# Kernel tuning notes

Hardware: AMD Instinct MI355X
Metric: run time of the kernel (lower is better)

## Reference

```python
import jax, jax.numpy as jnp
import numpy as np

# Dims matching init_kwargs: k=5, inplanes=512, planes=512, m=4, padding=None, stride=1
N, C, H, W = 32, 512, 56, 56
M = 4
CM = C // M          # 128, = group count (depthwise)
K1 = 5               # dynamic kernel size
K2 = 3               # atrous kernel size (dilation 2)
P2 = 512 // 2        # planes // 2


def setup_inputs() -> dict:
    key = jax.random.key(0)
    ks = jax.random.split(key, 13)
    s = lambda i, shape: jax.random.normal(ks[i], shape, jnp.float32) * 0.05
    return dict(
        x=jax.random.normal(ks[0], (N, C, H, W), jnp.float32),
        W_conv=s(1, (CM, C)), b_conv=s(2, (CM,)),        # self.conv (1x1)
        wk=s(3, (K1 * K1,)), bk=s(4, (K1 * K1,)),        # self.conv_kernel (1->k*k, 1x1)
        wck=s(5, ()), bck=s(6, ()),                      # self.conv_k (1->1, 1x1 scalar affine)
        wk2=s(7, (K2 * K2,)), bk2=s(8, (K2 * K2,)),      # self.conv_kernel2 (1->9)
        wck2=s(9, ()), bck2=s(10, ()),                   # self.conv_k2
        W_fuse=s(11, (P2, CM)), b_fuse=s(12, (P2,)),     # self.fuse (1x1)
    )


def _dw_conv(f, kern, dil, pad):
    # Per-sample depthwise conv: fold batch into groups -> single conv call.
    # f: [N, CM, H, W], kern: [N, CM, k, k]
    n, cm, h, w = f.shape
    fr = f.reshape(1, n * cm, h, w)
    kr = kern.reshape(n * cm, 1, kern.shape[-2], kern.shape[-1])
    o = jax.lax.conv_general_dilated(
        fr, kr, window_strides=(1, 1), padding=[(pad, pad), (pad, pad)],
        rhs_dilation=(dil, dil), feature_group_count=n * cm,
        dimension_numbers=('NCHW', 'OIHW', 'NCHW'))
    return o.reshape(n, cm, h, w)


def reference(x, W_conv, b_conv, wk, bk, wck, bck, wk2, bk2, wck2, bck2, W_fuse, b_fuse):
    # f = relu(conv(x));  g = relu(conv(avg_pool(x)))
    f = jax.nn.relu(jnp.einsum('nchw,oc->nohw', x, W_conv) + b_conv[None, :, None, None])
    g = jax.nn.relu(x.mean((2, 3)) @ W_conv.T + b_conv)  # [N, CM]
    # dynamic per-channel kernels: (g*wk + bk)*wck + bck, reshaped to [N, CM, k, k]
    kern1 = ((g[:, :, None] * wk + bk) * wck + bck).reshape(N, CM, K1, K1)
    kern2 = ((g[:, :, None] * wk2 + bk2) * wck2 + bck2).reshape(N, CM, K2, K2)
    o1 = _dw_conv(f, kern1, dil=1, pad=(K1 - 1) // 2)   # plain branch
    o2 = _dw_conv(f, kern2, dil=2, pad=2)               # atrous branch
    y1 = jnp.einsum('nchw,oc->nohw', o1, W_fuse) + b_fuse[None, :, None, None]
    y2 = jnp.einsum('nchw,oc->nohw', o2, W_fuse) + b_fuse[None, :, None, None]
    return jnp.concatenate([y1, y2], axis=1)  # [N, planes, H, W]
```

## Files before the change

kernel.cpp:

```cpp
#include <hip/hip_runtime.h>

typedef unsigned short u16;
typedef unsigned int   u32;

#define NB   32
#define CIN  512
#define CM   128
#define P2   256
#define HW   3136
#define HD   56

typedef __attribute__((ext_vector_type(8))) short           short8;
typedef __attribute__((ext_vector_type(8))) unsigned short  ushort8;
typedef __attribute__((ext_vector_type(4))) unsigned short  ushort4_t;
typedef __attribute__((ext_vector_type(4))) float           f32x4;

__device__ __forceinline__ float b2f(u16 u) {
    union { u32 i; float f; } v; v.i = ((u32)u) << 16; return v.f;
}
__device__ __forceinline__ u16 f2b(float f) {
    u32 u = __builtin_bit_cast(u32, f);
    u32 r = (u + 0x7fffu + ((u >> 16) & 1u)) >> 16;
    return (u16)r;
}

__global__ __launch_bounds__(256) void init_kernel(const float* __restrict__ Wc,
                                                   const float* __restrict__ Wf,
                                                   u16* __restrict__ Wcb,
                                                   u16* __restrict__ Wfb,
                                                   float* __restrict__ xm) {
    int i = blockIdx.x * 256 + threadIdx.x;
    if (i < CM * CIN) { Wcb[i] = f2b(Wc[i]); return; }
    i -= CM * CIN;
    if (i < P2 * CM) { Wfb[i] = f2b(Wf[i]); return; }
    i -= P2 * CM;
    if (i < NB * CIN) xm[i] = 0.f;
}

__global__ __launch_bounds__(128) void g_kernel(const float* __restrict__ Wc,
                                                const float* __restrict__ bc,
                                                const float* __restrict__ xm,
                                                float* __restrict__ g) {
    const int n = blockIdx.x, cm = threadIdx.x;
    __shared__ float xs[CIN];
    for (int i = threadIdx.x; i < CIN; i += 128)
        xs[i] = xm[n * CIN + i] * (1.0f / HW);
    __syncthreads();
    const float* wrow = Wc + (size_t)cm * CIN;
    float acc = 0.f;
    for (int c = 0; c < CIN; ++c) acc += wrow[c] * xs[c];
    acc += bc[cm];
    g[n * CM + cm] = fmaxf(acc, 0.f);
}

template<int IN_F32, int OUT_F32, int RELU, int MEAN, int TWOBR>
__global__ __launch_bounds__(256) void gemm_kernel(
    const void* __restrict__ In0, const void* __restrict__ In1,
    const u16* __restrict__ Wm, const float* __restrict__ bias,
    void* __restrict__ Out, float* __restrict__ xm,
    int K, int ch_stride)
{
    __shared__ u16 ldsT[128 * 36];

    int n, ch_off;
    const void* In;
    if (TWOBR) {
        n      = blockIdx.z >> 1;
        int br = blockIdx.z & 1;
        In     = br ? In1 : In0;
        ch_off = br ? P2 : 0;
    } else {
        n = blockIdx.z; In = In0; ch_off = 0;
    }
    const int hw0  = blockIdx.x * 128;
    const int mblk = blockIdx.y * 128;
    const int tid  = threadIdx.x;
    const int wave = tid >> 6, lane = tid & 63;
    const int wm   = (wave >> 1) * 64;
    const int wn   = (wave & 1) * 64;
    const int qa   = lane >> 4;
    const int l15  = lane & 15;

    f32x4 acc[4][4] = {};

    const int kpair = tid >> 4;
    const int c0    = (tid & 15) * 8;
    const int hwc   = hw0 + c0;
    const bool cok  = (hwc < HW);

    for (int k0 = 0; k0 < K; k0 += 32) {
        __syncthreads();
        u32 pk[8];
        if (IN_F32) {
            f32x4 a0 = {0,0,0,0}, a1 = {0,0,0,0}, d0 = {0,0,0,0}, d1 = {0,0,0,0};
            if (cok) {
                const float* p0 = (const float*)In + (size_t)n * K * HW
                                + (size_t)(k0 + kpair * 2) * HW + hwc;
                a0 = *(const f32x4*)p0;
                a1 = *(const f32x4*)(p0 + 4);
                d0 = *(const f32x4*)(p0 + HW);
                d1 = *(const f32x4*)(p0 + HW + 4);
            }
            float fa[8] = {a0[0],a0[1],a0[2],a0[3],a1[0],a1[1],a1[2],a1[3]};
            float fb[8] = {d0[0],d0[1],d0[2],d0[3],d1[0],d1[1],d1[2],d1[3]};
            #pragma unroll
            for (int e = 0; e < 8; ++e) {
                u32 ua = __builtin_bit_cast(u32, fa[e]) + 0x8000u;
                u32 ub = __builtin_bit_cast(u32, fb[e]) + 0x8000u;
                pk[e] = __builtin_amdgcn_perm(ub, ua, 0x07060302u);
            }
            if (MEAN) {
                float s0 = fa[0]+fa[1]+fa[2]+fa[3]+fa[4]+fa[5]+fa[6]+fa[7];
                float s1 = fb[0]+fb[1]+fb[2]+fb[3]+fb[4]+fb[5]+fb[6]+fb[7];
                #pragma unroll
                for (int off = 8; off > 0; off >>= 1) {
                    s0 += __shfl_xor(s0, off, 16);
                    s1 += __shfl_xor(s1, off, 16);
                }
                if ((tid & 15) == 0) {
                    atomicAdd(&xm[n * CIN + k0 + kpair * 2],     s0);
                    atomicAdd(&xm[n * CIN + k0 + kpair * 2 + 1], s1);
                }
            }
        } else {
            ushort8 v0 = {0,0,0,0,0,0,0,0}, v1 = {0,0,0,0,0,0,0,0};
            if (cok) {
                const u16* p0 = (const u16*)In + (size_t)n * K * HW
                              + (size_t)(k0 + kpair * 2) * HW + hwc;
                v0 = *(const ushort8*)p0;
                v1 = *(const ushort8*)(p0 + HW);
            }
            #pragma unroll
            for (int e = 0; e < 8; ++e)
                pk[e] = (u32)v0[e] | ((u32)v1[e] << 16);
        }
        #pragma unroll
        for (int e = 0; e < 8; ++e)
            *(u32*)&ldsT[(c0 + e) * 36 + kpair * 2] = pk[e];
        __syncthreads();

        short8 a[4];
        #pragma unroll
        for (int mt = 0; mt < 4; ++mt) {
            int row = mblk + wm + mt * 16 + l15;
            a[mt] = *(const short8*)(Wm + (size_t)row * K + k0 + qa * 8);
        }
        #pragma unroll
        for (int nt = 0; nt < 4; ++nt) {
            int c = wn + nt * 16 + l15;
            union { ushort4_t h[2]; short8 v; } bu;
            bu.h[0] = *(const ushort4_t*)&ldsT[c * 36 + qa * 8];
            bu.h[1] = *(const ushort4_t*)&ldsT[c * 36 + qa * 8 + 4];
            short8 b = bu.v;
            #pragma unroll
            for (int mt = 0; mt < 4; ++mt)
                acc[mt][nt] = __builtin_amdgcn_mfma_f32_16x16x32_bf16(a[mt], b, acc[mt][nt], 0, 0, 0);
        }
    }

    const int r4 = qa * 4;
    #pragma unroll
    for (int nt = 0; nt < 4; ++nt) {
        int colhw = hw0 + wn + nt * 16 + l15;
        if (colhw >= HW) continue;
        #pragma unroll
        for (int mt = 0; mt < 4; ++mt) {
            int mbase = mblk + wm + mt * 16 + r4;
            #pragma unroll
            for (int r = 0; r < 4; ++r) {
                int m = mbase + r;
                float v = acc[mt][nt][r] + bias[m];
                if (RELU) v = fmaxf(v, 0.f);
                size_t idx = ((size_t)n * ch_stride + ch_off + m) * HW + colhw;
                if (OUT_F32) ((float*)Out)[idx] = v;
                else         ((u16*)Out)[idx]  = f2b(v);
            }
        }
    }
}

__global__ __launch_bounds__(256) void dw_kernel(
    const u16* __restrict__ f, const float* __restrict__ g,
    const float* __restrict__ wk,  const float* __restrict__ bk,
    const float* __restrict__ wck, const float* __restrict__ bck,
    const float* __restrict__ wk2, const float* __restrict__ bk2,
    const float* __restrict__ wck2,const float* __restrict__ bck2,
    u16* __restrict__ o1, u16* __restrict__ o2)
{
    const int ncm = blockIdx.x;
    __shared__ float fpl[HW];
    __shared__ float kc1[25], kc2[9];

    const size_t base = (size_t)ncm * HW;
    const u32* fp = (const u32*)(f + base);
    for (int i = threadIdx.x; i < HW / 2; i += 256) {
        u32 v = fp[i];
        fpl[2 * i]     = b2f((u16)v);
        fpl[2 * i + 1] = b2f((u16)(v >> 16));
    }

    const float gv = g[ncm];
    if (threadIdx.x < 25) {
        int t = threadIdx.x;
        kc1[t] = (gv * wk[t] + bk[t]) * wck[0] + bck[0];
    } else if (threadIdx.x >= 32 && threadIdx.x < 41) {
        int t = threadIdx.x - 32;
        kc2[t] = (gv * wk2[t] + bk2[t]) * wck2[0] + bck2[0];
    }
    __syncthreads();

    u32* o1p = (u32*)(o1 + base);
    u32* o2p = (u32*)(o2 + base);
    for (int p2v = threadIdx.x; p2v < HW / 2; p2v += 256) {
        int px = p2v * 2;
        int h = px / HD, w = px - h * HD;
        float a1[2] = {0.f, 0.f}, a2[2] = {0.f, 0.f};
        #pragma unroll
        for (int i = 0; i < 5; ++i) {
            int hh = h + i - 2; if (hh < 0 || hh >= HD) continue;
            const float* row = &fpl[hh * HD];
            #pragma unroll
            for (int j = 0; j < 5; ++j) {
                float kv = kc1[i * 5 + j];
                int w0 = w + j - 2;
                if (w0 >= 0 && w0 < HD) a1[0] += kv * row[w0];
                int w1 = w0 + 1;
                if (w1 >= 0 && w1 < HD) a1[1] += kv * row[w1];
            }
        }
        #pragma unroll
        for (int i = 0; i < 3; ++i) {
            int hh = h + (i - 1) * 2; if (hh < 0 || hh >= HD) continue;
            const float* row = &fpl[hh * HD];
            #pragma unroll
            for (int j = 0; j < 3; ++j) {
                float kv = kc2[i * 3 + j];
                int w0 = w + (j - 1) * 2;
                if (w0 >= 0 && w0 < HD) a2[0] += kv * row[w0];
                int w1 = w0 + 1;
                if (w1 >= 0 && w1 < HD) a2[1] += kv * row[w1];
            }
        }
        o1p[p2v] = (u32)f2b(a1[0]) | ((u32)f2b(a1[1]) << 16);
        o2p[p2v] = (u32)f2b(a2[0]) | ((u32)f2b(a2[1]) << 16);
    }
}

extern "C" void kernel_launch(void* const* d_in, const int* in_sizes, int n_in,
                              void* d_out, int out_size, void* d_ws, size_t ws_size,
                              hipStream_t stream) {
    const float* x     = (const float*)d_in[0];
    const float* Wconv = (const float*)d_in[1];
    const float* bconv = (const float*)d_in[2];
    const float* wk    = (const float*)d_in[3];
    const float* bk    = (const float*)d_in[4];
    const float* wck   = (const float*)d_in[5];
    const float* bck   = (const float*)d_in[6];
    const float* wk2   = (const float*)d_in[7];
    const float* bk2   = (const float*)d_in[8];
    const float* wck2  = (const float*)d_in[9];
    const float* bck2  = (const float*)d_in[10];
    const float* Wfuse = (const float*)d_in[11];
    const float* bfuse = (const float*)d_in[12];
    float* out = (float*)d_out;

    float* xm  = (float*)d_ws;
    float* g   = xm + NB * CIN;
    u16*   Wcb = (u16*)(g + NB * CM);
    u16*   Wfb = Wcb + CM * CIN;
    u16*   f   = Wfb + P2 * CM;
    u16*   o1  = f  + (size_t)NB * CM * HW;
    u16*   o2  = o1 + (size_t)NB * CM * HW;

    {
        int tot = CM * CIN + P2 * CM + NB * CIN;
        init_kernel<<<dim3((tot + 255) / 256), 256, 0, stream>>>(Wconv, Wfuse, Wcb, Wfb, xm);
    }
    gemm_kernel<1,0,1,1,0><<<dim3(25, 1, NB), 256, 0, stream>>>(
        x, nullptr, Wcb, bconv, f, xm, CIN, CM);
    g_kernel<<<dim3(NB), 128, 0, stream>>>(Wconv, bconv, xm, g);
    dw_kernel<<<dim3(NB * CM), 256, 0, stream>>>(f, g, wk, bk, wck, bck,
                                                 wk2, bk2, wck2, bck2, o1, o2);
    gemm_kernel<0,1,0,0,1><<<dim3(25, 2, 2 * NB), 256, 0, stream>>>(
        o1, o2, Wfb, bfuse, out, nullptr, CM, 512);
}
```

Before: 500.8 us.

## Pad depthwise tile in LDS, register-block 8 outputs, add dedicated fuse GEMM

The depthwise kernel now zero-pads the 56x56 plane into a 60x60 LDS tile, so the inner loops no longer need bounds checks. Each thread computes 8 adjacent outputs from a 12-wide register row and reuses the same rows for the atrous branch. The fuse GEMM becomes a dedicated kernel that loads the full K=128 slab into LDS once per 64-pixel tile, with all 256 output rows in one block per branch, replacing the templated K-loop GEMM. The first GEMM is de-templated with no functional change. This adds an LDS zero-fill and an extra sync in the depthwise kernel, and the fuse kernel now has smaller N tiles.

```diff
diff --git a/kernel.cpp b/kernel.cpp
--- a/kernel.cpp
+++ b/kernel.cpp
@@ -53,25 +53,14 @@
     g[n * CM + cm] = fmaxf(acc, 0.f);
 }
 
-template<int IN_F32, int OUT_F32, int RELU, int MEAN, int TWOBR>
-__global__ __launch_bounds__(256) void gemm_kernel(
-    const void* __restrict__ In0, const void* __restrict__ In1,
+__global__ __launch_bounds__(256) void gemm1_kernel(
+    const float* __restrict__ In,
     const u16* __restrict__ Wm, const float* __restrict__ bias,
-    void* __restrict__ Out, float* __restrict__ xm,
-    int K, int ch_stride)
+    u16* __restrict__ Out, float* __restrict__ xm)
 {
     __shared__ u16 ldsT[128 * 36];
 
-    int n, ch_off;
-    const void* In;
-    if (TWOBR) {
-        n      = blockIdx.z >> 1;
-        int br = blockIdx.z & 1;
-        In     = br ? In1 : In0;
-        ch_off = br ? P2 : 0;
-    } else {
-        n = blockIdx.z; In = In0; ch_off = 0;
-    }
+    const int n    = blockIdx.z;
     const int hw0  = blockIdx.x * 128;
     const int mblk = blockIdx.y * 128;
     const int tid  = threadIdx.x;
@@ -88,13 +77,13 @@
     const int hwc   = hw0 + c0;
     const bool cok  = (hwc < HW);
 
-    for (int k0 = 0; k0 < K; k0 += 32) {
+    for (int k0 = 0; k0 < CIN; k0 += 32) {
         __syncthreads();
         u32 pk[8];
-        if (IN_F32) {
+        {
             f32x4 a0 = {0,0,0,0}, a1 = {0,0,0,0}, d0 = {0,0,0,0}, d1 = {0,0,0,0};
             if (cok) {
-                const float* p0 = (const float*)In + (size_t)n * K * HW
+                const float* p0 = In + (size_t)n * CIN * HW
                                 + (size_t)(k0 + kpair * 2) * HW + hwc;
                 a0 = *(const f32x4*)p0;
                 a1 = *(const f32x4*)(p0 + 4);
@@ -109,30 +98,17 @@
                 u32 ub = __builtin_bit_cast(u32, fb[e]) + 0x8000u;
                 pk[e] = __builtin_amdgcn_perm(ub, ua, 0x07060302u);
             }
-            if (MEAN) {
-                float s0 = fa[0]+fa[1]+fa[2]+fa[3]+fa[4]+fa[5]+fa[6]+fa[7];
-                float s1 = fb[0]+fb[1]+fb[2]+fb[3]+fb[4]+fb[5]+fb[6]+fb[7];
-                #pragma unroll
-                for (int off = 8; off > 0; off >>= 1) {
-                    s0 += __shfl_xor(s0, off, 16);
-                    s1 += __shfl_xor(s1, off, 16);
-                }
-                if ((tid & 15) == 0) {
-                    atomicAdd(&xm[n * CIN + k0 + kpair * 2],     s0);
-                    atomicAdd(&xm[n * CIN + k0 + kpair * 2 + 1], s1);
-                }
-            }
-        } else {
-            ushort8 v0 = {0,0,0,0,0,0,0,0}, v1 = {0,0,0,0,0,0,0,0};
-            if (cok) {
-                const u16* p0 = (const u16*)In + (size_t)n * K * HW
-                              + (size_t)(k0 + kpair * 2) * HW + hwc;
-                v0 = *(const ushort8*)p0;
-                v1 = *(const ushort8*)(p0 + HW);
-            }
-            #pragma unroll
-            for (int e = 0; e < 8; ++e)
-                pk[e] = (u32)v0[e] | ((u32)v1[e] << 16);
+            float s0 = fa[0]+fa[1]+fa[2]+fa[3]+fa[4]+fa[5]+fa[6]+fa[7];
+            float s1 = fb[0]+fb[1]+fb[2]+fb[3]+fb[4]+fb[5]+fb[6]+fb[7];
+            #pragma unroll
+            for (int off = 8; off > 0; off >>= 1) {
+                s0 += __shfl_xor(s0, off, 16);
+                s1 += __shfl_xor(s1, off, 16);
+            }
+            if ((tid & 15) == 0) {
+                atomicAdd(&xm[n * CIN + k0 + kpair * 2],     s0);
+                atomicAdd(&xm[n * CIN + k0 + kpair * 2 + 1], s1);
+            }
         }
         #pragma unroll
         for (int e = 0; e < 8; ++e)
@@ -143,7 +119,7 @@
         #pragma unroll
         for (int mt = 0; mt < 4; ++mt) {
             int row = mblk + wm + mt * 16 + l15;
-            a[mt] = *(const short8*)(Wm + (size_t)row * K + k0 + qa * 8);
+            a[mt] = *(const short8*)(Wm + (size_t)row * CIN + k0 + qa * 8);
         }
         #pragma unroll
         for (int nt = 0; nt < 4; ++nt) {
@@ -169,16 +145,14 @@
             #pragma unroll
             for (int r = 0; r < 4; ++r) {
                 int m = mbase + r;
-                float v = acc[mt][nt][r] + bias[m];
-                if (RELU) v = fmaxf(v, 0.f);
-                size_t idx = ((size_t)n * ch_stride + ch_off + m) * HW + colhw;
-                if (OUT_F32) ((float*)Out)[idx] = v;
-                else         ((u16*)Out)[idx]  = f2b(v);
-            }
-        }
-    }
-}
-
+                float v = fmaxf(acc[mt][nt][r] + bias[m], 0.f);
+                Out[((size_t)n * CM + m) * HW + colhw] = f2b(v);
+            }
+        }
+    }
+}
+
+#define PD 60
 __global__ __launch_bounds__(256) void dw_kernel(
     const u16* __restrict__ f, const float* __restrict__ g,
     const float* __restrict__ wk,  const float* __restrict__ bk,
@@ -188,17 +162,14 @@
     u16* __restrict__ o1, u16* __restrict__ o2)
 {
     const int ncm = blockIdx.x;
-    __shared__ float fpl[HW];
+    __shared__ float fpl[PD * PD];
     __shared__ float kc1[25], kc2[9];
 
-    const size_t base = (size_t)ncm * HW;
-    const u32* fp = (const u32*)(f + base);
-    for (int i = threadIdx.x; i < HW / 2; i += 256) {
-        u32 v = fp[i];
-        fpl[2 * i]     = b2f((u16)v);
-        fpl[2 * i + 1] = b2f((u16)(v >> 16));
-    }
-
+    {
+        f32x4 z = {0.f, 0.f, 0.f, 0.f};
+        f32x4* fv = (f32x4*)fpl;
+        for (int i = threadIdx.x; i < PD * PD / 4; i += 256) fv[i] = z;
+    }
     const float gv = g[ncm];
     if (threadIdx.x < 25) {
         int t = threadIdx.x;
@@ -209,40 +180,124 @@
     }
     __syncthreads();
 
+    const size_t base = (size_t)ncm * HW;
+    const u32* fp = (const u32*)(f + base);
+    for (int i = threadIdx.x; i < HW / 2; i += 256) {
+        u32 v = fp[i];
+        int px = 2 * i;
+        int h = px / HD, w = px - h * HD;
+        float* dst = &fpl[(h + 2) * PD + (w + 2)];
+        dst[0] = b2f((u16)v);
+        dst[1] = b2f((u16)(v >> 16));
+    }
+    __syncthreads();
+
     u32* o1p = (u32*)(o1 + base);
     u32* o2p = (u32*)(o2 + base);
-    for (int p2v = threadIdx.x; p2v < HW / 2; p2v += 256) {
-        int px = p2v * 2;
-        int h = px / HD, w = px - h * HD;
-        float a1[2] = {0.f, 0.f}, a2[2] = {0.f, 0.f};
-        #pragma unroll
-        for (int i = 0; i < 5; ++i) {
-            int hh = h + i - 2; if (hh < 0 || hh >= HD) continue;
-            const float* row = &fpl[hh * HD];
+    for (int u = threadIdx.x; u < 392; u += 256) {
+        int h  = u / 7;
+        int gq = u - h * 7;
+        int w0 = gq * 8;
+        float a1[8] = {}, a2[8] = {};
+        #pragma unroll
+        for (int di = 0; di < 5; ++di) {
+            const float* row = &fpl[(h + di) * PD + w0];
+            float r[12];
+            #pragma unroll
+            for (int x = 0; x < 12; ++x) r[x] = row[x];
             #pragma unroll
             for (int j = 0; j < 5; ++j) {
-                float kv = kc1[i * 5 + j];
-                int w0 = w + j - 2;
-                if (w0 >= 0 && w0 < HD) a1[0] += kv * row[w0];
-                int w1 = w0 + 1;
-                if (w1 >= 0 && w1 < HD) a1[1] += kv * row[w1];
-            }
-        }
-        #pragma unroll
-        for (int i = 0; i < 3; ++i) {
-            int hh = h + (i - 1) * 2; if (hh < 0 || hh >= HD) continue;
-            const float* row = &fpl[hh * HD];
-            #pragma unroll
-            for (int j = 0; j < 3; ++j) {
-                float kv = kc2[i * 3 + j];
-                int w0 = w + (j - 1) * 2;
-                if (w0 >= 0 && w0 < HD) a2[0] += kv * row[w0];
-                int w1 = w0 + 1;
-                if (w1 >= 0 && w1 < HD) a2[1] += kv * row[w1];
-            }
-        }
-        o1p[p2v] = (u32)f2b(a1[0]) | ((u32)f2b(a1[1]) << 16);
-        o2p[p2v] = (u32)f2b(a2[0]) | ((u32)f2b(a2[1]) << 16);
+                float kv = kc1[di * 5 + j];
+                #pragma unroll
+                for (int e = 0; e < 8; ++e) a1[e] = fmaf(kv, r[j + e], a1[e]);
+            }
+            if ((di & 1) == 0) {
+                int i2 = di >> 1;
+                #pragma unroll
+                for (int j = 0; j < 3; ++j) {
+                    float kv = kc2[i2 * 3 + j];
+                    #pragma unroll
+                    for (int e = 0; e < 8; ++e) a2[e] = fmaf(kv, r[2 * j + e], a2[e]);
+                }
+            }
+        }
+        int ob = (h * HD + w0) >> 1;
+        #pragma unroll
+        for (int e = 0; e < 4; ++e) {
+            o1p[ob + e] = (u32)f2b(a1[2 * e]) | ((u32)f2b(a1[2 * e + 1]) << 16);
+            o2p[ob + e] = (u32)f2b(a2[2 * e]) | ((u32)f2b(a2[2 * e + 1]) << 16);
+        }
+    }
+}
+
+#define FSTR 140
+__global__ __launch_bounds__(256) void fuse_kernel(
+    const u16* __restrict__ o1, const u16* __restrict__ o2,
+    const u16* __restrict__ Wfb, const float* __restrict__ bias,
+    float* __restrict__ out)
+{
+    __shared__ u16 ldsT[64 * FSTR];
+
+    const int n   = blockIdx.z;
+    const int br  = blockIdx.y;
+    const u16* In = br ? o2 : o1;
+    const int ch_off = br ? P2 : 0;
+    const int hw0 = blockIdx.x * 64;
+    const int tid = threadIdx.x;
+    const int wave = tid >> 6, lane = tid & 63;
+    const int wm  = wave * 64;
+    const int qa  = lane >> 4, l15 = lane & 15;
+
+    {
+        const int c0 = (tid & 7) * 8;
+        const int kp = tid >> 3;
+        #pragma unroll
+        for (int kk = 0; kk < CM; kk += 64) {
+            const u16* p0 = In + (size_t)n * CM * HW + (size_t)(kk + 2 * kp) * HW + hw0 + c0;
+            ushort8 v0 = *(const ushort8*)p0;
+            ushort8 v1 = *(const ushort8*)(p0 + HW);
+            #pragma unroll
+            for (int e = 0; e < 8; ++e)
+                *(u32*)&ldsT[(c0 + e) * FSTR + kk + 2 * kp] = (u32)v0[e] | ((u32)v1[e] << 16);
+        }
+    }
+    __syncthreads();
+
+    f32x4 acc[4][4] = {};
+    #pragma unroll
+    for (int q = 0; q < 4; ++q) {
+        short8 a[4];
+        #pragma unroll
+        for (int mt = 0; mt < 4; ++mt) {
+            int row = wm + mt * 16 + l15;
+            a[mt] = *(const short8*)(Wfb + (size_t)row * CM + q * 32 + qa * 8);
+        }
+        #pragma unroll
+        for (int nt = 0; nt < 4; ++nt) {
+            int c = nt * 16 + l15;
+            union { ushort4_t h[2]; short8 v; } bu;
+            bu.h[0] = *(const ushort4_t*)&ldsT[c * FSTR + q * 32 + qa * 8];
+            bu.h[1] = *(const ushort4_t*)&ldsT[c * FSTR + q * 32 + qa * 8 + 4];
+            #pragma unroll
+            for (int mt = 0; mt < 4; ++mt)
+                acc[mt][nt] = __builtin_amdgcn_mfma_f32_16x16x32_bf16(a[mt], bu.v, acc[mt][nt], 0, 0, 0);
+        }
+    }
+
+    const int r4 = qa * 4;
+    #pragma unroll
+    for (int nt = 0; nt < 4; ++nt) {
+        int colhw = hw0 + nt * 16 + l15;
+        #pragma unroll
+        for (int mt = 0; mt < 4; ++mt) {
+            int mbase = wm + mt * 16 + r4;
+            #pragma unroll
+            for (int r = 0; r < 4; ++r) {
+                int m = mbase + r;
+                float v = acc[mt][nt][r] + bias[m];
+                out[((size_t)n * 512 + ch_off + m) * HW + colhw] = v;
+            }
+        }
     }
 }
 
@@ -276,11 +331,9 @@
         int tot = CM * CIN + P2 * CM + NB * CIN;
         init_kernel<<<dim3((tot + 255) / 256), 256, 0, stream>>>(Wconv, Wfuse, Wcb, Wfb, xm);
     }
-    gemm_kernel<1,0,1,1,0><<<dim3(25, 1, NB), 256, 0, stream>>>(
-        x, nullptr, Wcb, bconv, f, xm, CIN, CM);
+    gemm1_kernel<<<dim3(25, 1, NB), 256, 0, stream>>>(x, Wcb, bconv, f, xm);
     g_kernel<<<dim3(NB), 128, 0, stream>>>(Wconv, bconv, xm, g);
     dw_kernel<<<dim3(NB * CM), 256, 0, stream>>>(f, g, wk, bk, wck, bck,
                                                  wk2, bk2, wck2, bck2, o1, o2);
-    gemm_kernel<0,1,0,0,1><<<dim3(25, 2, 2 * NB), 256, 0, stream>>>(
-        o1, o2, Wfb, bfuse, out, nullptr, CM, 512);
-}
+    fuse_kernel<<<dim3(49, 2, NB), 256, 0, stream>>>(o1, o2, Wfb, bfuse, out);
+}
```

Result: faster. 456.4 us (-8.9%).
